# Performance work log

Measured on AMD Instinct MI355X. Metric: run time of the kernel, lower is better.

Reference implementation:

```python
import jax, jax.numpy as jnp
import numpy as np

N_HEADS = 16


def setup_inputs() -> dict:
    key = jax.random.key(0)
    ks = jax.random.split(key, 4)
    B, S, E = 4, 2048, 1024
    x = jax.random.normal(ks[0], (B, S, E), dtype=jnp.float32)
    w_attn = jax.random.normal(ks[1], (E, 3 * E), dtype=jnp.float32) * 0.02
    b_attn = jnp.zeros((3 * E,), dtype=jnp.float32)
    w_proj = jax.random.normal(ks[2], (E, E), dtype=jnp.float32) * 0.02
    b_proj = jnp.zeros((E,), dtype=jnp.float32)
    return {"x": x, "w_attn": w_attn, "b_attn": b_attn, "w_proj": w_proj, "b_proj": b_proj}


def reference(x, w_attn, b_attn, w_proj, b_proj):
    B, S, E = x.shape
    H = N_HEADS
    D = E // H
    # fused QKV projection (Conv1D: x @ W + b)
    qkv = x @ w_attn + b_attn                     # [B, S, 3E]
    q, k, v = jnp.split(qkv, 3, axis=-1)          # each [B, S, E]
    q = q.reshape(B, S, H, D).transpose(0, 2, 1, 3)  # [B, H, S, D]
    k = k.reshape(B, S, H, D).transpose(0, 2, 1, 3)
    v = v.reshape(B, S, H, D).transpose(0, 2, 1, 3)
    # scaled QK^T
    scores = jnp.einsum('bhqd,bhkd->bhqk', q, k) / jnp.sqrt(jnp.asarray(D, dtype=x.dtype))
    # causal mask via where with dtype-min fill (matches torch.where(c_m, w, finfo.min))
    causal = jnp.tril(jnp.ones((S, S), dtype=bool))  # [S, S]
    scores = jnp.where(causal[None, None, :, :], scores, jnp.finfo(scores.dtype).min)
    attn = jax.nn.softmax(scores, axis=-1)        # [B, H, S, S]
    o = jnp.einsum('bhqk,bhkd->bhqd', attn, v)    # [B, H, S, D]
    o = o.transpose(0, 2, 1, 3).reshape(B, S, E)  # merge heads
    return o @ w_proj + b_proj                    # output projection
```

## Files before the change

### kernel.cpp

```cpp
#include <hip/hip_runtime.h>
#include <stdint.h>


typedef __bf16 bf16;
typedef __bf16 bf16x4 __attribute__((ext_vector_type(4)));
typedef __bf16 bf16x8 __attribute__((ext_vector_type(8)));
typedef float  f32x4  __attribute__((ext_vector_type(4)));

#define DEV __device__ __forceinline__

DEV void async_copy16(bf16* lds, const bf16* g) {
  __builtin_amdgcn_global_load_lds(
      (__attribute__((address_space(1))) void*)(uintptr_t)g,
      (__attribute__((address_space(3))) void*)(uint32_t)(uintptr_t)lds,
      16, 0, 0);
}

__global__ __launch_bounds__(256) void cast_x_kernel(const float* __restrict__ in,
                                                     bf16* __restrict__ out, int n4) {
  int i = blockIdx.x * blockDim.x + threadIdx.x;
  int stride = gridDim.x * blockDim.x;
  for (; i < n4; i += stride) {
    float4 v = ((const float4*)in)[i];
    bf16x4 o = { (bf16)v.x, (bf16)v.y, (bf16)v.z, (bf16)v.w };
    *(bf16x4*)(out + (size_t)i * 4) = o;
  }
}

__global__ __launch_bounds__(256) void transpose_cast_kernel(const float* __restrict__ W,
                                                             bf16* __restrict__ Wt,
                                                             int Kd, int Nd) {
  __shared__ alignas(16) bf16 T[64 * 80];
  const int t = threadIdx.x;
  const int n0 = blockIdx.x * 64;
  const int k0 = blockIdx.y * 64;
#pragma unroll
  for (int i = 0; i < 4; ++i) {
    int idx = t + i * 256;
    int r  = idx >> 4;
    int c4 = (idx & 15) * 4;
    float4 v = *(const float4*)(W + (size_t)(k0 + r) * Nd + n0 + c4);
    bf16x4 o = { (bf16)v.x, (bf16)v.y, (bf16)v.z, (bf16)v.w };
    *(bf16x4*)(&T[r * 80 + c4]) = o;
  }
  __syncthreads();
#pragma unroll
  for (int i = 0; i < 2; ++i) {
    int idx = t + i * 256;
    int n = idx >> 3;
    int c = idx & 7;
    bf16x8 o;
#pragma unroll
    for (int j = 0; j < 8; ++j) o[j] = T[(c * 8 + j) * 80 + n];
    *(bf16x8*)(Wt + (size_t)(n0 + n) * Kd + k0 + c * 8) = o;
  }
}

__global__ __launch_bounds__(256) void vtrans_kernel(const bf16* __restrict__ qkv,
                                                     bf16* __restrict__ vt) {
  __shared__ alignas(16) bf16 T[64 * 80];
  const int t  = threadIdx.x;
  const int s0 = blockIdx.x * 64;
  const int bh = blockIdx.y;
  const int b = bh >> 4, h = bh & 15;
#pragma unroll
  for (int i = 0; i < 2; ++i) {
    int idx = t + i * 256;
    int s = idx >> 3, c = idx & 7;
    bf16x8 v = *(const bf16x8*)(qkv + (size_t)(b * 2048 + s0 + s) * 3072 + 2048 + h * 64 + c * 8);
    *(bf16x8*)(&T[s * 80 + c * 8]) = v;
  }
  __syncthreads();
#pragma unroll
  for (int i = 0; i < 2; ++i) {
    int idx = t + i * 256;
    int d = idx >> 3, c = idx & 7;
    bf16x8 o;
#pragma unroll
    for (int j = 0; j < 8; ++j) o[j] = T[(c * 8 + j) * 80 + d];
    *(bf16x8*)(vt + (size_t)(bh * 64 + d) * 2048 + s0 + c * 8) = o;
  }
}

template <typename OutT>
__global__ __launch_bounds__(512, 2) void gemm256_kernel(const bf16* __restrict__ A,
                                                         const bf16* __restrict__ Bt,
                                                         const float* __restrict__ bias,
                                                         OutT* __restrict__ C,
                                                         int M, int N, int K,
                                                         float qscale, int qcols,
                                                         int nbx) {
  __shared__ alignas(16) bf16 As[3][256 * 64];
  __shared__ alignas(16) bf16 Bs[3][128 * 64];

  const int tid  = threadIdx.x;
  const int lane = tid & 63;
  const int w    = tid >> 6;
  const int wm = w >> 1, wn = w & 1;
  const int l15 = lane & 15, l16 = lane >> 4;

  const int nwg = (int)gridDim.x;
  const int cpx = nwg >> 3;
  const int swz = ((int)blockIdx.x & 7) * cpx + ((int)blockIdx.x >> 3);
  const int m0 = (swz / nbx) * 256;
  const int n0 = (swz % nbx) * 128;

  const int srow = tid >> 3;
  const int sc   = tid & 7;
#define STAGE_HALF(buf, kt, H)                                                  \
  {                                                                             \
    const int k0_ = (kt) * 64;                                                  \
    _Pragma("unroll")                                                           \
    for (int j = 2 * (H); j < 2 * (H) + 2; ++j) {                               \
      int row = j * 64 + srow;                                                  \
      const bf16* src = A + (size_t)(m0 + row) * K + k0_ + 8 * (sc ^ (row & 7));\
      async_copy16(&As[buf][(j * 512 + w * 64) * 8], src);                      \
    }                                                                           \
    {                                                                           \
      int row = (H) * 64 + srow;                                                \
      const bf16* src = Bt + (size_t)(n0 + row) * K + k0_ + 8 * (sc ^ (row & 7));\
      async_copy16(&Bs[buf][((H) * 512 + w * 64) * 8], src);                    \
    }                                                                           \
  }

  f32x4 acc[4][4];
  f32x4 zf = {0.f, 0.f, 0.f, 0.f};
#pragma unroll
  for (int i = 0; i < 4; ++i)
#pragma unroll
    for (int j = 0; j < 4; ++j) acc[i][j] = zf;

  const int KT = K >> 6;
  STAGE_HALF(0, 0, 0) STAGE_HALF(0, 0, 1)
  STAGE_HALF(1, 1, 0) STAGE_HALF(1, 1, 1)

#define MFMA_HALF(buf, MLO)                                                     \
  {                                                                             \
    __builtin_amdgcn_s_setprio(1);                                              \
    _Pragma("unroll")                                                           \
    for (int m = (MLO); m < (MLO) + 2; ++m) {                                   \
      int ra = wm * 64 + m * 16 + l15;                                          \
      bf16x8 a0 = *(const bf16x8*)(&As[buf][ra * 64 + 8 * ((0 + l16) ^ (ra & 7))]); \
      bf16x8 a1 = *(const bf16x8*)(&As[buf][ra * 64 + 8 * ((4 + l16) ^ (ra & 7))]); \
      _Pragma("unroll")                                                         \
      for (int n = 0; n < 4; ++n)                                               \
        acc[m][n] = __builtin_amdgcn_mfma_f32_16x16x32_bf16(a0, bfr[n][0], acc[m][n], 0, 0, 0); \
      _Pragma("unroll")                                                         \
      for (int n = 0; n < 4; ++n)                                               \
        acc[m][n] = __builtin_amdgcn_mfma_f32_16x16x32_bf16(a1, bfr[n][1], acc[m][n], 0, 0, 0); \
    }                                                                           \
    __builtin_amdgcn_s_setprio(0);                                              \
  }

  int bufc = 0;
  int bufs = 2;
  for (int kt = 0; kt < KT - 1; ++kt) {
    asm volatile("s_waitcnt vmcnt(6)" ::: "memory");
    __builtin_amdgcn_s_barrier();
    asm volatile("" ::: "memory");
    const bool st = (kt + 2 < KT);
    if (st) STAGE_HALF(bufs, kt + 2, 0)
    bf16x8 bfr[4][2];
#pragma unroll
    for (int n = 0; n < 4; ++n) {
      int rb = wn * 64 + n * 16 + l15;
#pragma unroll
      for (int kk = 0; kk < 2; ++kk)
        bfr[n][kk] = *(const bf16x8*)(&Bs[bufc][rb * 64 + 8 * ((kk * 4 + l16) ^ (rb & 7))]);
    }
    MFMA_HALF(bufc, 0)
    asm volatile("" ::: "memory");
    __builtin_amdgcn_s_barrier();
    asm volatile("" ::: "memory");
    if (st) STAGE_HALF(bufs, kt + 2, 1)
    MFMA_HALF(bufc, 2)
    asm volatile("" ::: "memory");
    bufc = (bufc == 2) ? 0 : bufc + 1;
    bufs = (bufs == 2) ? 0 : bufs + 1;
  }
  asm volatile("s_waitcnt vmcnt(0)" ::: "memory");
  __builtin_amdgcn_s_barrier();
  asm volatile("" ::: "memory");
  {
    bf16x8 bfr[4][2];
#pragma unroll
    for (int n = 0; n < 4; ++n) {
      int rb = wn * 64 + n * 16 + l15;
#pragma unroll
      for (int kk = 0; kk < 2; ++kk)
        bfr[n][kk] = *(const bf16x8*)(&Bs[bufc][rb * 64 + 8 * ((kk * 4 + l16) ^ (rb & 7))]);
    }
    MFMA_HALF(bufc, 0)
    MFMA_HALF(bufc, 2)
  }

#pragma unroll
  for (int n = 0; n < 4; ++n) {
    int col = n0 + wn * 64 + n * 16 + l15;
    float bb = bias[col];
    float sc2 = (col < qcols) ? qscale : 1.0f;
#pragma unroll
    for (int m = 0; m < 4; ++m) {
#pragma unroll
      for (int reg = 0; reg < 4; ++reg) {
        int row = m0 + wm * 64 + m * 16 + l16 * 4 + reg;
        C[(size_t)row * N + col] = (OutT)((acc[m][n][reg] + bb) * sc2);
      }
    }
  }
#undef STAGE_HALF
#undef MFMA_HALF
}

__global__ __launch_bounds__(512, 4) void flash_kernel(const bf16* __restrict__ qkv,
                                                       const bf16* __restrict__ vt,
                                                       bf16* __restrict__ obuf) {
  constexpr int S = 2048, E3 = 3072;
  __shared__ alignas(16) bf16 Ks[2][64 * 64];
  __shared__ alignas(16) bf16 Vs[2][64 * 64];
  __shared__ alignas(16) bf16 Ps[8][16 * 64];

  const int tid  = threadIdx.x;
  const int lane = tid & 63;
  const int w    = tid >> 6;
  const int bx = blockIdx.x;
  const int bh = blockIdx.y;
  const int b = bh >> 4, h = bh & 15;
  const int l15 = lane & 15, l16 = lane >> 4;

  const int sr  = w * 8 + (lane >> 3);
  const int scc = lane & 7;
  const bf16* kstage = qkv + (size_t)(b * S + sr) * E3 + 1024 + h * 64 + 8 * (scc ^ (sr & 7));
  const bf16* vstage = vt + (size_t)(bh * 64 + sr) * S + 8 * (scc ^ (sr & 7));

  const int xsw = l15 & 7;
  const uint32_t rdA = (uint32_t)(l15 * 128 + 16 * (l16 ^ xsw));
  const uint32_t rdB = (uint32_t)(l15 * 128 + 16 * ((4 + l16) ^ xsw));
  const uint32_t wbase = (uint32_t)(w * 2048);
  uint32_t pwo[4];
#pragma unroll
  for (int kf = 0; kf < 4; ++kf)
    pwo[kf] = wbase + (uint32_t)(l15 * 128 + (((kf * 2) | (l16 >> 1)) ^ xsw) * 16 + (l16 & 1) * 8);
  const uint32_t pr0 = wbase + rdA, pr1 = wbase + rdB;

#define KV_STAGE(buf, kv0_)                                        \
  {                                                                \
    async_copy16(Ks[buf] + w * 512, kstage + (size_t)(kv0_) * E3); \
    async_copy16(Vs[buf] + w * 512, vstage + (kv0_));              \
  }

  for (int half = 0; half < 2; ++half) {
    const int t = half ? (15 - bx) : bx;
    const int q0 = t * 128;
    const int wq0 = q0 + w * 16;
    const int nsteps = 2 * t + 2;

    KV_STAGE(0, 0)

    bf16x8 qf[2];
    {
      const bf16* qbase = qkv + (size_t)(b * S + wq0 + l15) * E3 + h * 64;
#pragma unroll
      for (int dk = 0; dk < 2; ++dk)
        qf[dk] = *(const bf16x8*)(qbase + (dk * 4 + l16) * 8);
    }

    float lstate = 0.f;
    f32x4 oacc[4];
    f32x4 zf = {0.f, 0.f, 0.f, 0.f};
#pragma unroll
    for (int i = 0; i < 4; ++i) oacc[i] = zf;

    __syncthreads();

#define FLASH_STEP(CUR, STEPIDX)                                                  \
    {                                                                             \
      const int kv0 = (STEPIDX) * 64;                                             \
      if ((STEPIDX) + 1 < nsteps) KV_STAGE((CUR) ^ 1, kv0 + 64)                   \
      if (kv0 <= wq0 + 15) {                     \
        f32x4 sv[4];                                                              \
        _Pragma("unroll")                                                         \
        for (int kf = 0; kf < 4; ++kf) sv[kf] = zf;                               \
        __builtin_amdgcn_s_setprio(1);                                            \
        _Pragma("unroll")                                                         \
        for (int kf = 0; kf < 4; ++kf) {                                          \
          bf16x8 k0 = *(const bf16x8*)((const char*)Ks[CUR] + rdA + kf * 2048);   \
          sv[kf] = __builtin_amdgcn_mfma_f32_16x16x32_bf16(k0, qf[0], sv[kf], 0, 0, 0); \
          bf16x8 k1 = *(const bf16x8*)((const char*)Ks[CUR] + rdB + kf * 2048);   \
          sv[kf] = __builtin_amdgcn_mfma_f32_16x16x32_bf16(k1, qf[1], sv[kf], 0, 0, 0); \
        }                                                                         \
        __builtin_amdgcn_s_setprio(0);                                            \
        if (kv0 + 63 > wq0) {     \
          const int qrow_ = wq0 + l15;                                            \
          _Pragma("unroll")                                                       \
          for (int kf = 0; kf < 4; ++kf)                                          \
            _Pragma("unroll")                                                     \
            for (int reg = 0; reg < 4; ++reg) {                                   \
              int key = kv0 + kf * 16 + l16 * 4 + reg;                            \
              if (key > qrow_) sv[kf][reg] = -1e30f;                              \
            }                                                                     \
        }                                                                         \
        float rsum = 0.f;                                                         \
        _Pragma("unroll")                                                         \
        for (int kf = 0; kf < 4; ++kf) {                                          \
          _Pragma("unroll")                                                       \
          for (int reg = 0; reg < 4; ++reg) {                                     \
            float p = __builtin_amdgcn_exp2f(sv[kf][reg]);                        \
            sv[kf][reg] = p;                                                      \
            rsum += p;                                                            \
          }                                                                       \
          bf16x4 quad = { (bf16)sv[kf][0], (bf16)sv[kf][1],                       \
                          (bf16)sv[kf][2], (bf16)sv[kf][3] };                     \
          *(bf16x4*)((char*)Ps + pwo[kf]) = quad;                                 \
        }                                                                         \
        rsum += __shfl_xor(rsum, 16);                                             \
        rsum += __shfl_xor(rsum, 32);                                             \
        lstate += rsum;                                                           \
        bf16x8 pb0 = *(const bf16x8*)((const char*)Ps + pr0);                     \
        bf16x8 pb1 = *(const bf16x8*)((const char*)Ps + pr1);                     \
        __builtin_amdgcn_s_setprio(1);                                            \
        _Pragma("unroll")                                                         \
        for (int nf = 0; nf < 4; ++nf) {                                          \
          bf16x8 vf0 = *(const bf16x8*)((const char*)Vs[CUR] + rdA + nf * 2048);  \
          oacc[nf] = __builtin_amdgcn_mfma_f32_16x16x32_bf16(vf0, pb0, oacc[nf], 0, 0, 0); \
          bf16x8 vf1 = *(const bf16x8*)((const char*)Vs[CUR] + rdB + nf * 2048);  \
          oacc[nf] = __builtin_amdgcn_mfma_f32_16x16x32_bf16(vf1, pb1, oacc[nf], 0, 0, 0); \
        }                                                                         \
        __builtin_amdgcn_s_setprio(0);                                            \
      }                                                                           \
      __syncthreads();          \
    }

    for (int step = 0; step < nsteps; step += 2) {
      FLASH_STEP(0, step)
      FLASH_STEP(1, step + 1)
    }
#undef FLASH_STEP

    float inv = 1.0f / lstate;
    int qrow = wq0 + l15;
#pragma unroll
    for (int nf = 0; nf < 4; ++nf) {
      bf16x4 o4 = { (bf16)(oacc[nf][0] * inv), (bf16)(oacc[nf][1] * inv),
                    (bf16)(oacc[nf][2] * inv), (bf16)(oacc[nf][3] * inv) };
      *(bf16x4*)(obuf + (size_t)(b * S + qrow) * 1024 + h * 64 + nf * 16 + l16 * 4) = o4;
    }
  }
#undef KV_STAGE
}

extern "C" void kernel_launch(void* const* d_in, const int* in_sizes, int n_in,
                              void* d_out, int out_size, void* d_ws, size_t ws_size,
                              hipStream_t stream) {
  (void)in_sizes; (void)n_in; (void)out_size; (void)ws_size;
  const float* x      = (const float*)d_in[0];
  const float* w_attn = (const float*)d_in[1];
  const float* b_attn = (const float*)d_in[2];
  const float* w_proj = (const float*)d_in[3];
  const float* b_proj = (const float*)d_in[4];
  float* out = (float*)d_out;

  char* ws = (char*)d_ws;
  bf16* xb  = (bf16*)(ws + 0);
  bf16* wat = (bf16*)(ws + 16777216);
  bf16* wpt = (bf16*)(ws + 23068672);
  bf16* qkv = (bf16*)(ws + 25165824);
  bf16* vt  = (bf16*)(ws + 75497472);
  bf16* ob  = (bf16*)(ws + 92274688);

  const float QSCALE = 0.18033688011112042f;

  cast_x_kernel<<<2048, 256, 0, stream>>>(x, xb, 8192 * 1024 / 4);
  transpose_cast_kernel<<<dim3(48, 16), 256, 0, stream>>>(w_attn, wat, 1024, 3072);
  transpose_cast_kernel<<<dim3(16, 16), 256, 0, stream>>>(w_proj, wpt, 1024, 1024);
  gemm256_kernel<bf16><<<768, 512, 0, stream>>>(xb, wat, b_attn, qkv,
                                                8192, 3072, 1024, QSCALE, 1024, 24);
  vtrans_kernel<<<dim3(32, 64), 256, 0, stream>>>(qkv, vt);
  flash_kernel<<<dim3(8, 64), 512, 0, stream>>>(qkv, vt, ob);
  gemm256_kernel<float><<<256, 512, 0, stream>>>(ob, wpt, b_proj, out,
                                                 8192, 1024, 1024, 1.0f, 0, 8);
}
```

Measured before the change: 169.8 us.

## Keep softmax P in registers by permuting V^T key order

The flash kernel no longer writes P to LDS and reads it back as an MFMA operand. Instead, the V transpose kernel stores keys in a permuted order that matches the register layout of the QK^T accumulator, so P can be packed directly from registers into bf16x8 operands. This removes the per-step LDS round trip and its shared buffer, which frees LDS and may raise occupancy. The cost is a nonstandard V^T layout that only this kernel understands and must stay consistent with the MFMA fragment mapping.

Result: faster. 163.6 us (-3.6%).

```diff
diff --git a/kernel.cpp b/kernel.cpp
--- a/kernel.cpp
+++ b/kernel.cpp
@@ -77,7 +77,11 @@
     int d = idx >> 3, c = idx & 7;
     bf16x8 o;
 #pragma unroll
-    for (int j = 0; j < 8; ++j) o[j] = T[(c * 8 + j) * 80 + d];
+    for (int j = 0; j < 8; ++j) {
+      int pos = c * 8 + j;
+      int key = (pos & 32) | (((pos >> 2) & 1) << 4) | (((pos >> 3) & 3) << 2) | (pos & 3);
+      o[j] = T[key * 80 + d];
+    }
     *(bf16x8*)(vt + (size_t)(bh * 64 + d) * 2048 + s0 + c * 8) = o;
   }
 }
@@ -218,7 +222,6 @@
   constexpr int S = 2048, E3 = 3072;
   __shared__ alignas(16) bf16 Ks[2][64 * 64];
   __shared__ alignas(16) bf16 Vs[2][64 * 64];
-  __shared__ alignas(16) bf16 Ps[8][16 * 64];
 
   const int tid  = threadIdx.x;
   const int lane = tid & 63;
@@ -236,12 +239,6 @@
   const int xsw = l15 & 7;
   const uint32_t rdA = (uint32_t)(l15 * 128 + 16 * (l16 ^ xsw));
   const uint32_t rdB = (uint32_t)(l15 * 128 + 16 * ((4 + l16) ^ xsw));
-  const uint32_t wbase = (uint32_t)(w * 2048);
-  uint32_t pwo[4];
-#pragma unroll
-  for (int kf = 0; kf < 4; ++kf)
-    pwo[kf] = wbase + (uint32_t)(l15 * 128 + (((kf * 2) | (l16 >> 1)) ^ xsw) * 16 + (l16 & 1) * 8);
-  const uint32_t pr0 = wbase + rdA, pr1 = wbase + rdB;
 
 #define KV_STAGE(buf, kv0_)                                        \
   {                                                                \
@@ -302,29 +299,34 @@
         }                                                                         \
         float rsum = 0.f;                                                         \
         _Pragma("unroll")                                                         \
-        for (int kf = 0; kf < 4; ++kf) {                                          \
+        for (int kf = 0; kf < 4; ++kf)                                            \
           _Pragma("unroll")                                                       \
           for (int reg = 0; reg < 4; ++reg) {                                     \
             float p = __builtin_amdgcn_exp2f(sv[kf][reg]);                        \
             sv[kf][reg] = p;                                                      \
             rsum += p;                                                            \
           }                                                                       \
-          bf16x4 quad = { (bf16)sv[kf][0], (bf16)sv[kf][1],                       \
-                          (bf16)sv[kf][2], (bf16)sv[kf][3] };                     \
-          *(bf16x4*)((char*)Ps + pwo[kf]) = quad;                                 \
-        }                                                                         \
         rsum += __shfl_xor(rsum, 16);                                             \
         rsum += __shfl_xor(rsum, 32);                                             \
         lstate += rsum;                                                           \
-        bf16x8 pb0 = *(const bf16x8*)((const char*)Ps + pr0);                     \
-        bf16x8 pb1 = *(const bf16x8*)((const char*)Ps + pr1);                     \
+             \
+        bf16x8 pb[2];                                                             \
+        _Pragma("unroll")                                                         \
+        for (int kc = 0; kc < 2; ++kc) {                                          \
+          bf16x8 tq;                                                              \
+          tq[0] = (bf16)sv[2 * kc][0];  tq[1] = (bf16)sv[2 * kc][1];              \
+          tq[2] = (bf16)sv[2 * kc][2];  tq[3] = (bf16)sv[2 * kc][3];              \
+          tq[4] = (bf16)sv[2 * kc + 1][0]; tq[5] = (bf16)sv[2 * kc + 1][1];       \
+          tq[6] = (bf16)sv[2 * kc + 1][2]; tq[7] = (bf16)sv[2 * kc + 1][3];       \
+          pb[kc] = tq;                                                            \
+        }                                                                         \
         __builtin_amdgcn_s_setprio(1);                                            \
         _Pragma("unroll")                                                         \
         for (int nf = 0; nf < 4; ++nf) {                                          \
           bf16x8 vf0 = *(const bf16x8*)((const char*)Vs[CUR] + rdA + nf * 2048);  \
-          oacc[nf] = __builtin_amdgcn_mfma_f32_16x16x32_bf16(vf0, pb0, oacc[nf], 0, 0, 0); \
+          oacc[nf] = __builtin_amdgcn_mfma_f32_16x16x32_bf16(vf0, pb[0], oacc[nf], 0, 0, 0); \
           bf16x8 vf1 = *(const bf16x8*)((const char*)Vs[CUR] + rdB + nf * 2048);  \
-          oacc[nf] = __builtin_amdgcn_mfma_f32_16x16x32_bf16(vf1, pb1, oacc[nf], 0, 0, 0); \
+          oacc[nf] = __builtin_amdgcn_mfma_f32_16x16x32_bf16(vf1, pb[1], oacc[nf], 0, 0, 0); \
         }                                                                         \
         __builtin_amdgcn_s_setprio(0);                                            \
       }                                                                           \
```
